# Optimization experiments

Hardware: AMD Instinct MI355X
Metric: run time of the kernel (lower is better)

## Reference

```python
import jax, jax.numpy as jnp
import numpy as np

N_U, N_I, D = 8192, 8192, 128


def setup_inputs() -> dict:
    key = jax.random.key(0)
    k1, k2, k3, k4, k5 = jax.random.split(key, 5)
    h_u = jax.random.normal(k1, (N_U, D), dtype=jnp.float32)
    h_i = jax.random.normal(k2, (N_I, D), dtype=jnp.float32)
    ui_adj = jax.random.randint(k3, (N_U, N_I), 0, 2).astype(jnp.int32)
    # learned params: W is nn.Linear(d, d, bias=False) -> weight [d, d]; a is [2d]
    W = jax.random.normal(k4, (D, D), dtype=jnp.float32) * (1.0 / np.sqrt(D))
    a = jax.random.normal(k5, (2 * D,), dtype=jnp.float32) * 0.1
    return {"h_u": h_u, "h_i": h_i, "ui_adj": ui_adj, "W": W, "a": a}


def reference(h_u, h_i, ui_adj, W, a):
    # torch nn.Linear: x @ W.T
    Wu = h_u @ W.T                      # [N_u, d]
    Wi = h_i @ W.T                      # [N_i, d]
    d = Wu.shape[1]
    a1 = Wu @ a[:d]                     # [N_u]
    a2 = Wi @ a[d:]                     # [N_i]
    e = jax.nn.leaky_relu(a1[:, None] + a2[None, :], negative_slope=0.2)  # [N_u, N_i]
    adj = ui_adj != 0
    no_item = ~adj.any(axis=-1)         # rows with zero neighbors
    e = jnp.where(adj, e, -jnp.inf)
    # avoid all -inf rows (torch softmax -> NaN -> nan_to_num -> 0); use 0 logits then zero alpha
    e = jnp.where(no_item[:, None], 0.0, e)
    alpha = jax.nn.softmax(e, axis=-1)  # [N_u, N_i]
    alpha = jnp.where(no_item[:, None], 0.0, alpha)
    out = alpha @ Wi                    # [N_u, d]
    out = jnp.where(no_item[:, None], 0.0, out)
    return (out, alpha)
```

## Files before the change

kernel.cpp:

```cpp
#include <hip/hip_runtime.h>

#define NU 8192
#define NI 8192
#define DD 128

typedef float fx4 __attribute__((ext_vector_type(4)));
typedef int   ix4 __attribute__((ext_vector_type(4)));
typedef short bx8 __attribute__((ext_vector_type(8)));
typedef short sx4 __attribute__((ext_vector_type(4)));

__device__ __forceinline__ short f2bf(float f) {
  unsigned u = __float_as_uint(f);
  u = (u + 0x7FFFu + ((u >> 16) & 1u)) >> 16;
  return (short)u;
}
__device__ __forceinline__ float lrelu(float x) { return fmaxf(x, 0.2f * x); }

__global__ __launch_bounds__(256) void k_prep(
    const float* __restrict__ hU, const float* __restrict__ hI,
    const float* __restrict__ W, const float* __restrict__ a,
    float* __restrict__ a1, float* __restrict__ e1, float* __restrict__ e2,
    short* __restrict__ WiT, float* __restrict__ blkmax)
{
  __shared__ float Wl[128 * 128];
  __shared__ float vv[2][128];
  __shared__ float red[64];
  const int tid = threadIdx.x;
#pragma unroll
  for (int it = 0; it < 16; ++it) {
    int idx = it * 1024 + tid * 4;
    *(fx4*)(Wl + idx) = *(const fx4*)(W + idx);
  }
  __syncthreads();
  if (tid < 128) {
    float s1 = 0.f, s2 = 0.f;
    for (int k = 0; k < DD; ++k) {
      float w = Wl[k * 128 + tid];
      s1 += a[k] * w;
      s2 += a[DD + k] * w;
    }
    vv[0][tid] = s1; vv[1][tid] = s2;
  }
  __syncthreads();

  const int i0 = blockIdx.x * 64;
  {
    const int rg = tid & 15;
    const int kg = tid >> 4;
    const int r0 = i0 + rg * 4;
    const int k0 = kg * 8;
    float acc[4][8];
#pragma unroll
    for (int r = 0; r < 4; ++r)
#pragma unroll
      for (int c = 0; c < 8; ++c) acc[r][c] = 0.f;
    for (int j = 0; j < 128; j += 4) {
      fx4 wv8[8], hv[4];
#pragma unroll
      for (int c = 0; c < 8; ++c) wv8[c] = *(const fx4*)(Wl + (k0 + c) * 128 + j);
#pragma unroll
      for (int r = 0; r < 4; ++r) hv[r] = *(const fx4*)(hI + (size_t)(r0 + r) * DD + j);
#pragma unroll
      for (int r = 0; r < 4; ++r)
#pragma unroll
        for (int c = 0; c < 8; ++c)
          acc[r][c] += hv[r][0]*wv8[c][0] + hv[r][1]*wv8[c][1] + hv[r][2]*wv8[c][2] + hv[r][3]*wv8[c][3];
    }
#pragma unroll
    for (int c = 0; c < 8; ++c) {
      sx4 pk;
#pragma unroll
      for (int r = 0; r < 4; ++r) pk[r] = f2bf(acc[r][c]);
      *(sx4*)(WiT + (size_t)(k0 + c) * NI + r0) = pk;
    }
  }

  if (tid < 64) {
    const int row = i0 + tid;
    const fx4* hv = (const fx4*)(hU + (size_t)row * DD);
    const fx4* vq = (const fx4*)&vv[0][0];
    float s = 0.f;
#pragma unroll
    for (int q = 0; q < DD / 4; ++q) {
      fx4 hq = hv[q], vqq = vq[q];
      s += hq[0]*vqq[0] + hq[1]*vqq[1] + hq[2]*vqq[2] + hq[3]*vqq[3];
    }
    a1[row] = s;
  } else if (tid < 128) {
    const int row = i0 + (tid - 64);
    const fx4* hv = (const fx4*)(hI + (size_t)row * DD);
    const fx4* vq = (const fx4*)&vv[1][0];
    float s = 0.f;
#pragma unroll
    for (int q = 0; q < DD / 4; ++q) {
      fx4 hq = hv[q], vqq = vq[q];
      s += hq[0]*vqq[0] + hq[1]*vqq[1] + hq[2]*vqq[2] + hq[3]*vqq[3];
    }
    e1[row] = __expf(s);
    e2[row] = __expf(0.2f * s);
    red[tid - 64] = s;
  }
  __syncthreads();
  if (tid < 32) red[tid] = fmaxf(red[tid], red[tid + 32]);
  __syncthreads();
  if (tid < 16) red[tid] = fmaxf(red[tid], red[tid + 16]);
  __syncthreads();
  if (tid < 8)  red[tid] = fmaxf(red[tid], red[tid + 8]);
  __syncthreads();
  if (tid < 4)  red[tid] = fmaxf(red[tid], red[tid + 4]);
  __syncthreads();
  if (tid == 0)
    blkmax[blockIdx.x] = fmaxf(fmaxf(red[0], red[1]), fmaxf(red[2], red[3]));
}

__global__ void k_mx(const float* __restrict__ blkmax, float* __restrict__ mx) {
  __shared__ float r[128];
  const int tid = threadIdx.x;
  r[tid] = blkmax[tid];
  __syncthreads();
  for (int s = 64; s > 0; s >>= 1) {
    if (tid < s) r[tid] = fmaxf(r[tid], r[tid + s]);
    __syncthreads();
  }
  if (tid == 0) mx[0] = r[0];
}

__global__ __launch_bounds__(256, 4) void k_fuseA(
    const int* __restrict__ adj, const float* __restrict__ a1g,
    const float* __restrict__ e1g, const float* __restrict__ e2g,
    const float* __restrict__ mxp,
    fx4* __restrict__ kcons, unsigned* __restrict__ mask,
    float* __restrict__ alphap)
{
  const int row  = blockIdx.x;
  const int tid  = threadIdx.x;
  const int lane = tid & 63;
  const int wv   = tid >> 6;
  const size_t base = (size_t)row * NI;
  ix4 m[8];
#pragma unroll
  for (int q = 0; q < 8; ++q)
    m[q] = __builtin_nontemporal_load((const ix4*)(adj + base + q * 1024 + tid * 4));
  const float A  = a1g[row];
  const float C  = lrelu(A + mxp[0]);
  const float K1 = __expf(A - C);
  const float K2 = __expf(0.2f * A - C);
  const float T1 = __expf(-A);
  fx4 p[8];
  float ps = 0.f;
#pragma unroll
  for (int q = 0; q < 8; ++q) {
    const int i0 = q * 1024 + tid * 4;
    const fx4 E1 = *(const fx4*)(e1g + i0);
    const fx4 E2 = *(const fx4*)(e2g + i0);
    unsigned long long b[4];
#pragma unroll
    for (int e = 0; e < 4; ++e) {
      const bool mm  = (m[q][e] != 0);
      const bool sel = (E1[e] > T1);
      const float val = sel ? E1[e] * K1 : E2[e] * K2;
      const float pv  = mm ? val : 0.f;
      p[q][e] = pv;
      ps += pv;
      b[e] = __ballot(mm);
    }
    if (lane < 8) {
      unsigned w = 0u;
#pragma unroll
      for (int e = 0; e < 4; ++e) {
        unsigned x = (unsigned)((b[e] >> (lane * 8)) & 0xFFull);
        x = (x | (x << 12)) & 0x000F000Fu;
        x = (x | (x << 6))  & 0x03030303u;
        x = (x | (x << 3))  & 0x11111111u;
        w |= x << e;
      }
      mask[(size_t)row * 256 + q * 32 + wv * 8 + lane] = w;
    }
  }
#pragma unroll
  for (int st = 1; st < 64; st <<= 1) ps += __shfl_xor(ps, st, 64);
  __shared__ float lp[4];
  if (lane == 0) lp[wv] = ps;
  __syncthreads();
  const float l  = lp[0] + lp[1] + lp[2] + lp[3];
  const float ri = (l > 0.f) ? (1.f / l) : 0.f;
#pragma unroll
  for (int q = 0; q < 8; ++q) {
    fx4 o;
#pragma unroll
    for (int e = 0; e < 4; ++e) o[e] = p[q][e] * ri;
    *(fx4*)(alphap + base + q * 1024 + tid * 4) = o;
  }
  if (tid == 0) kcons[row] = (fx4){K1 * ri, K2 * ri, T1, ri};
}

__global__ __launch_bounds__(512, 4) void k_gemm(
    const unsigned* __restrict__ mask, const fx4* __restrict__ kcons,
    const float* __restrict__ e1g, const float* __restrict__ e2g,
    const short* __restrict__ WiT, float* __restrict__ partial)
{
  __shared__ __align__(16) char lds[32768];
  const int tid  = threadIdx.x;
  const int lane = tid & 63;
  const int wv   = tid >> 6;
  const int wm   = wv & 3;
  const int wn2  = wv >> 2;
  const int uTile = (int)blockIdx.x >> 2;
  const int quar  = (int)blockIdx.x & 3;
  const int u0 = uTile * 64;
  const int ib = quar * 2048;
  const int lr = lane & 15, lg = lane >> 4;

  const int rowm = u0 + wm * 16 + lr;
  const fx4 kcm = kcons[rowm];
  const float K1m = kcm[0], K2m = kcm[1], T1m = kcm[2];
  const unsigned* mrow = mask + (size_t)rowm * 256 + quar * 64;

  const int sd = tid >> 3;
  const int si = tid & 7;
  const short* g0 = WiT + (size_t)sd * NI + ib + si * 8;
  const short* g1 = WiT + (size_t)(sd + 64) * NI + ib + si * 8;
  const int swz = (si * 16) ^ ((sd & 7) << 4);
  const int w0 = sd * 128 + swz;
  const int w1 = (sd + 64) * 128 + swz;

  fx4 acc[4];
#pragma unroll
  for (int n = 0; n < 4; ++n) acc[n] = (fx4){0.f, 0.f, 0.f, 0.f};

  bx8 sA = *(const bx8*)g0;
  bx8 sB = *(const bx8*)g1;
  *(bx8*)(lds + w0) = sA;
  *(bx8*)(lds + w1) = sB;

  for (int c = 0; c < 32; ++c) {
    char* buf = lds + (c & 1) * 16384;
    const int nxt = ((c + 1) & 1) * 16384;
    if (c < 31) {
      sA = *(const bx8*)(g0 + (c + 1) * 64);
      sB = *(const bx8*)(g1 + (c + 1) * 64);
    }
    __syncthreads();

#pragma unroll
    for (int ks = 0; ks < 2; ++ks) {
      const int ksg = c * 2 + ks;
      const unsigned by = (mrow[ksg] >> (lg * 8)) & 0xFFu;
      const int io = ksg * 32 + lg * 8;
      const fx4 e1a = *(const fx4*)(e1g + ib + io);
      const fx4 e1b = *(const fx4*)(e1g + ib + io + 4);
      const fx4 e2a = *(const fx4*)(e2g + ib + io);
      const fx4 e2b = *(const fx4*)(e2g + ib + io + 4);
      bx8 af;
#pragma unroll
      for (int j = 0; j < 8; ++j) {
        const float e1v = (j < 4) ? e1a[j] : e1b[j - 4];
        const float e2v = (j < 4) ? e2a[j] : e2b[j - 4];
        const float val = (e1v > T1m) ? e1v * K1m : e2v * K2m;
        af[j] = ((by >> j) & 1u) ? f2bf(val) : (short)0;
      }
#pragma unroll
      for (int nf = 0; nf < 4; ++nf) {
        const int d = wn2 * 64 + nf * 16 + lr;
        const bx8 bf = *(const bx8*)(buf + d * 128 +
                        ((ks * 64 + lg * 16) ^ ((lr & 7) << 4)));
        acc[nf] = __builtin_amdgcn_mfma_f32_16x16x32_bf16(af, bf, acc[nf], 0, 0, 0);
      }
    }

    if (c < 31) {
      *(bx8*)(lds + nxt + w0) = sA;
      *(bx8*)(lds + nxt + w1) = sB;
    }
  }

  float* pb = partial + (size_t)blockIdx.x * (64 * 128);
#pragma unroll
  for (int nf = 0; nf < 4; ++nf)
#pragma unroll
    for (int v = 0; v < 4; ++v)
      pb[(wm * 16 + lg * 4 + v) * 128 + wn2 * 64 + nf * 16 + lr] = acc[nf][v];
}

__global__ __launch_bounds__(512) void k_comb(
    const float* __restrict__ partial, float* __restrict__ outp)
{
  const int g = blockIdx.x * 512 + threadIdx.x;
  const int u = g >> 5;
  const int c4 = (g & 31) * 4;
  const int uTile = u >> 6, r = u & 63;
  const float* p0 = partial + ((size_t)uTile * 4) * 8192 + r * 128 + c4;
  fx4 s = *(const fx4*)p0;
#pragma unroll
  for (int q = 1; q < 4; ++q) {
    fx4 t = *(const fx4*)(p0 + (size_t)q * 8192);
    s[0] += t[0]; s[1] += t[1]; s[2] += t[2]; s[3] += t[3];
  }
  *(fx4*)(outp + (size_t)u * DD + c4) = s;
}

extern "C" void kernel_launch(void* const* d_in, const int* in_sizes, int n_in,
                              void* d_out, int out_size, void* d_ws, size_t ws_size,
                              hipStream_t stream) {
  (void)in_sizes; (void)n_in; (void)out_size; (void)ws_size;
  const float* h_u = (const float*)d_in[0];
  const float* h_i = (const float*)d_in[1];
  const int*   adj = (const int*)d_in[2];
  const float* W   = (const float*)d_in[3];
  const float* a   = (const float*)d_in[4];

  float* outp   = (float*)d_out;
  float* alphap = (float*)d_out + (size_t)NU * DD;

  char* ws = (char*)d_ws;
  float*    mx     = (float*)(ws + 1024);
  float*    blkmax = (float*)(ws + 2048);
  float*    a1     = (float*)(ws + 4096);
  float*    e1t    = (float*)(ws + 102400);
  float*    e2t    = (float*)(ws + 135168);
  short*    WiT    = (short*)(ws + 262144);
  unsigned* mask   = (unsigned*)(ws + 2359296);
  float*    part   = (float*)(ws + 11534336);
  fx4*      kcons  = (fx4*)(ws + 29360128);

  k_prep  <<<128,  256, 0, stream>>>(h_u, h_i, W, a, a1, e1t, e2t, WiT, blkmax);
  k_mx    <<<1,    128, 0, stream>>>(blkmax, mx);
  k_fuseA <<<NU,   256, 0, stream>>>(adj, a1, e1t, e2t, mx, kcons, mask, alphap);
  k_gemm  <<<512,  512, 0, stream>>>(mask, kcons, e1t, e2t, WiT, part);
  k_comb  <<<512,  512, 0, stream>>>(part, outp);
}
```

Before: 203.4 us.

## Split GEMM waves across K instead of N, widen fuseA blocks, nontemporal alpha stores

k_fuseA now runs 512 threads per row with 4 chunks each and writes alpha with nontemporal stores to avoid polluting cache with the large output. k_gemm's waves are reassigned so the two wave groups split the K dimension (each takes one 32-wide k-step per chunk) and each wave covers all 128 output columns. This halves redundant A-fragment construction (mask/exp/bf16 conversion) per wave, at the cost of an LDS reduction between the two K halves at the end and twice the accumulator registers.

```diff
diff --git a/kernel.cpp b/kernel.cpp
--- a/kernel.cpp
+++ b/kernel.cpp
@@ -125,7 +125,7 @@
   if (tid == 0) mx[0] = r[0];
 }
 
-__global__ __launch_bounds__(256, 4) void k_fuseA(
+__global__ __launch_bounds__(512, 4) void k_fuseA(
     const int* __restrict__ adj, const float* __restrict__ a1g,
     const float* __restrict__ e1g, const float* __restrict__ e2g,
     const float* __restrict__ mxp,
@@ -137,20 +137,20 @@
   const int lane = tid & 63;
   const int wv   = tid >> 6;
   const size_t base = (size_t)row * NI;
-  ix4 m[8];
-#pragma unroll
-  for (int q = 0; q < 8; ++q)
-    m[q] = __builtin_nontemporal_load((const ix4*)(adj + base + q * 1024 + tid * 4));
+  ix4 m[4];
+#pragma unroll
+  for (int q = 0; q < 4; ++q)
+    m[q] = __builtin_nontemporal_load((const ix4*)(adj + base + q * 2048 + tid * 4));
   const float A  = a1g[row];
   const float C  = lrelu(A + mxp[0]);
   const float K1 = __expf(A - C);
   const float K2 = __expf(0.2f * A - C);
   const float T1 = __expf(-A);
-  fx4 p[8];
+  fx4 p[4];
   float ps = 0.f;
 #pragma unroll
-  for (int q = 0; q < 8; ++q) {
-    const int i0 = q * 1024 + tid * 4;
+  for (int q = 0; q < 4; ++q) {
+    const int i0 = q * 2048 + tid * 4;
     const fx4 E1 = *(const fx4*)(e1g + i0);
     const fx4 E2 = *(const fx4*)(e2g + i0);
     unsigned long long b[4];
@@ -174,22 +174,23 @@
         x = (x | (x << 3))  & 0x11111111u;
         w |= x << e;
       }
-      mask[(size_t)row * 256 + q * 32 + wv * 8 + lane] = w;
+      mask[(size_t)row * 256 + q * 64 + wv * 8 + lane] = w;
     }
   }
 #pragma unroll
   for (int st = 1; st < 64; st <<= 1) ps += __shfl_xor(ps, st, 64);
-  __shared__ float lp[4];
+  __shared__ float lp[8];
   if (lane == 0) lp[wv] = ps;
   __syncthreads();
-  const float l  = lp[0] + lp[1] + lp[2] + lp[3];
+  const float l  = ((lp[0] + lp[1]) + (lp[2] + lp[3]))
+                 + ((lp[4] + lp[5]) + (lp[6] + lp[7]));
   const float ri = (l > 0.f) ? (1.f / l) : 0.f;
 #pragma unroll
-  for (int q = 0; q < 8; ++q) {
+  for (int q = 0; q < 4; ++q) {
     fx4 o;
 #pragma unroll
     for (int e = 0; e < 4; ++e) o[e] = p[q][e] * ri;
-    *(fx4*)(alphap + base + q * 1024 + tid * 4) = o;
+    __builtin_nontemporal_store(o, (fx4*)(alphap + base + q * 2048 + tid * 4));
   }
   if (tid == 0) kcons[row] = (fx4){K1 * ri, K2 * ri, T1, ri};
 }
@@ -204,7 +205,7 @@
   const int lane = tid & 63;
   const int wv   = tid >> 6;
   const int wm   = wv & 3;
-  const int wn2  = wv >> 2;
+  const int kk   = wv >> 2;
   const int uTile = (int)blockIdx.x >> 2;
   const int quar  = (int)blockIdx.x & 3;
   const int u0 = uTile * 64;
@@ -224,9 +225,9 @@
   const int w0 = sd * 128 + swz;
   const int w1 = (sd + 64) * 128 + swz;
 
-  fx4 acc[4];
-#pragma unroll
-  for (int n = 0; n < 4; ++n) acc[n] = (fx4){0.f, 0.f, 0.f, 0.f};
+  fx4 acc[8];
+#pragma unroll
+  for (int n = 0; n < 8; ++n) acc[n] = (fx4){0.f, 0.f, 0.f, 0.f};
 
   bx8 sA = *(const bx8*)g0;
   bx8 sB = *(const bx8*)g1;
@@ -242,9 +243,8 @@
     }
     __syncthreads();
 
-#pragma unroll
-    for (int ks = 0; ks < 2; ++ks) {
-      const int ksg = c * 2 + ks;
+    {
+      const int ksg = c * 2 + kk;
       const unsigned by = (mrow[ksg] >> (lg * 8)) & 0xFFu;
       const int io = ksg * 32 + lg * 8;
       const fx4 e1a = *(const fx4*)(e1g + ib + io);
@@ -260,10 +260,10 @@
         af[j] = ((by >> j) & 1u) ? f2bf(val) : (short)0;
       }
 #pragma unroll
-      for (int nf = 0; nf < 4; ++nf) {
-        const int d = wn2 * 64 + nf * 16 + lr;
+      for (int nf = 0; nf < 8; ++nf) {
+        const int d = nf * 16 + lr;
         const bx8 bf = *(const bx8*)(buf + d * 128 +
-                        ((ks * 64 + lg * 16) ^ ((lr & 7) << 4)));
+                        ((kk * 64 + lg * 16) ^ ((lr & 7) << 4)));
         acc[nf] = __builtin_amdgcn_mfma_f32_16x16x32_bf16(af, bf, acc[nf], 0, 0, 0);
       }
     }
@@ -274,12 +274,26 @@
     }
   }
 
-  float* pb = partial + (size_t)blockIdx.x * (64 * 128);
-#pragma unroll
-  for (int nf = 0; nf < 4; ++nf)
-#pragma unroll
-    for (int v = 0; v < 4; ++v)
-      pb[(wm * 16 + lg * 4 + v) * 128 + wn2 * 64 + nf * 16 + lr] = acc[nf][v];
+  __syncthreads();
+  float* red = (float*)lds;
+  if (kk == 0) {
+#pragma unroll
+    for (int nf = 0; nf < 8; ++nf)
+#pragma unroll
+      for (int v = 0; v < 4; ++v)
+        red[(wm * 16 + lg * 4 + v) * 128 + nf * 16 + lr] = acc[nf][v];
+  }
+  __syncthreads();
+  if (kk == 1) {
+    float* pb = partial + (size_t)blockIdx.x * (64 * 128);
+#pragma unroll
+    for (int nf = 0; nf < 8; ++nf)
+#pragma unroll
+      for (int v = 0; v < 4; ++v) {
+        const int idx = (wm * 16 + lg * 4 + v) * 128 + nf * 16 + lr;
+        pb[idx] = red[idx] + acc[nf][v];
+      }
+  }
 }
 
 __global__ __launch_bounds__(512) void k_comb(
@@ -325,7 +339,7 @@
 
   k_prep  <<<128,  256, 0, stream>>>(h_u, h_i, W, a, a1, e1t, e2t, WiT, blkmax);
   k_mx    <<<1,    128, 0, stream>>>(blkmax, mx);
-  k_fuseA <<<NU,   256, 0, stream>>>(adj, a1, e1t, e2t, mx, kcons, mask, alphap);
+  k_fuseA <<<NU,   512, 0, stream>>>(adj, a1, e1t, e2t, mx, kcons, mask, alphap);
   k_gemm  <<<512,  512, 0, stream>>>(mask, kcons, e1t, e2t, WiT, part);
   k_comb  <<<512,  512, 0, stream>>>(part, outp);
 }
```

After: 177.1 us. 12.9% less time.
